# Kernel optimization log

Measured on AMD Instinct MI355X. Metric: run time of the kernel, lower is better.

Reference implementation:

```python
import jax, jax.numpy as jnp
import numpy as np

NUM_CAV = 62000            # CAVs in the ragged batch
K = 3                      # past frames per object


def _counts():
    # deterministic ragged counts in [1, 31]; sum = 2000 * 496 = 992000 objects
    return ((np.arange(NUM_CAV) % 31) + 1).astype(np.int32)


def setup_inputs() -> dict:
    key = jax.random.key(0)
    k1, k2 = jax.random.split(key)
    counts = _counts()
    n_obj = int(counts.sum())  # 992000
    # [N, 3, 7] past 7-dof boxes; only [..., :2] (x, y) is used
    past_k_object_bbx = jax.random.normal(k1, (n_obj, K, 7), dtype=jnp.float32) * 10.0
    # strictly increasing timestamps per CAV so frame-to-frame dt != 0
    dt = jax.random.uniform(k2, (NUM_CAV, K), dtype=jnp.float32, minval=0.05, maxval=0.2)
    past_k_time_interval = jnp.cumsum(dt, axis=1).reshape(-1)  # flat, view(-1,3) compatible
    past_k_object_cav_num = jnp.asarray(counts)
    return {
        'past_k_object_bbx': past_k_object_bbx,
        'past_k_time_interval': past_k_time_interval,
        'past_k_object_cav_num': past_k_object_cav_num,
    }


def reference(past_k_object_bbx, past_k_time_interval, past_k_object_cav_num):
    # Faithful vectorization of extract_date_backup1 (j-indexed replicate loop ==
    # repeat_interleave of per-CAV time rows to per-object rows).
    n_obj = past_k_object_bbx.shape[0]
    # time grid per CAV, reversed so index -1 is the most recent frame
    td = jnp.flip(past_k_time_interval.reshape(-1, K), axis=1)        # [C, 3]
    coords = jnp.flip(past_k_object_bbx[:, :, :2], axis=1)           # [N, 3, 2]
    coords = coords - coords[:, -1:, :]                               # normalize to last frame
    # ragged row replication -> gather via cumulative offsets
    offsets = jnp.cumsum(past_k_object_cav_num)                       # [C]
    cav_idx = jnp.searchsorted(offsets, jnp.arange(n_obj), side='right')
    td_rep = td[cav_idx]                                              # [N, 3]
    td_norm = td_rep - td_rep[:, -1:]                                  # [N, 3]
    dt = td_rep[:, 1:] - td_rep[:, :-1]                                # [N, 2] (time_encode)
    distance = coords[:, 1:, :] - coords[:, :-1, :]                    # [N, 2, 2]
    speed = distance / dt[..., None]                                   # [N, 2, 2]
    obj_input = jnp.concatenate([distance, speed], axis=-1)[None]      # [1, N, 2, 4]
    # linear extrapolation of last motion to t = 0 (the 'query')
    last_len = td_norm[:, -1] - td_norm[:, -2]                          # [N]
    safe_len = jnp.where(last_len == 0, jnp.float32(1.0), last_len)
    extrap = coords[:, -1, :] + (coords[:, -1, :] - coords[:, -2, :]) * (-td_rep[:, -1:]) / safe_len[:, None]
    query = jnp.where((last_len == 0)[:, None], jnp.float32(0.0), extrap).reshape(1, n_obj, 1, 2)
    target_time_diff = -td_rep[:, -1]                                  # [N]
    time_encode = dt                                                   # [N, 2]
    return obj_input, query, time_encode, target_time_diff
```

## Files before the change

### kernel.cpp

```cpp
#include <hip/hip_runtime.h>
#include <limits.h>
#include <stdint.h>

#define SCAN_BS 256
#define OBJ_BS  256
#define SLAB_F  (OBJ_BS * 21)
#define SLAB_CH (SLAB_F / 256)

__device__ __forceinline__ void gload_lds16(const void* g, void* l) {
    __builtin_amdgcn_global_load_lds(
        (const __attribute__((address_space(1))) uint32_t*)g,
        (__attribute__((address_space(3))) uint32_t*)l, 16, 0, 0);
}

__global__ __launch_bounds__(SCAN_BS) void chunk_sum_kernel(
    const int* __restrict__ counts, int C, int* __restrict__ chunkSum) {

    __shared__ int ws[SCAN_BS / 64];
    const int tid  = threadIdx.x;
    const int lane = tid & 63;
    const int wid  = tid >> 6;
    const int gid  = blockIdx.x * SCAN_BS + tid;

    int v = (gid < C) ? counts[gid] : 0;
    #pragma unroll
    for (int o = 32; o > 0; o >>= 1) v += __shfl_down(v, o, 64);
    if (lane == 0) ws[wid] = v;
    __syncthreads();
    if (tid == 0) chunkSum[blockIdx.x] = ws[0] + ws[1] + ws[2] + ws[3];
}

__global__ __launch_bounds__(SCAN_BS) void scan_emit_kernel(
    const int* __restrict__ counts, const int* __restrict__ chunkSum,
    int C, int nb, int* __restrict__ offsets, int* __restrict__ blockCav) {

    __shared__ int cw[SCAN_BS / 64];
    __shared__ int wv[SCAN_BS / 64];

    const int tid  = threadIdx.x;
    const int lane = tid & 63;
    const int wid  = tid >> 6;
    const int b    = blockIdx.x;
    const int gid  = b * SCAN_BS + tid;

    int cs = 0;
    for (int j = tid; j < b; j += SCAN_BS) cs += chunkSum[j];
    #pragma unroll
    for (int o = 32; o > 0; o >>= 1) cs += __shfl_down(cs, o, 64);

    const int v = (gid < C) ? counts[gid] : 0;
    int inc = v;
    #pragma unroll
    for (int o = 1; o < 64; o <<= 1) {
        int t = __shfl_up(inc, o, 64);
        if (lane >= o) inc += t;
    }

    if (lane == 0)  cw[wid] = cs;
    if (lane == 63) wv[wid] = inc;
    __syncthreads();

    int base = 0;
    #pragma unroll
    for (int w = 0; w < SCAN_BS / 64; ++w) {
        base += cw[w];
        if (w < wid) base += wv[w];
    }

    if (gid < C) {
        const int end = base + inc;
        offsets[gid] = end;
        const int start = end - v;
        int s0 = ((start + OBJ_BS - 1) / OBJ_BS) * OBJ_BS;
        for (int s = s0; s < end; s += OBJ_BS) blockCav[s / OBJ_BS] = gid;
    }
}


__global__ __launch_bounds__(OBJ_BS) void motion_kernel(
    const float* __restrict__ bbx, const float* __restrict__ tint,
    const int* __restrict__ offsets, const int* __restrict__ blockCav,
    int C, int N, float* __restrict__ out) {

    __shared__ __align__(16) float sb[SLAB_F];
    __shared__ int   soff[OBJ_BS + 1];
    __shared__ float st[3 * (OBJ_BS + 1)];

    const int tid  = threadIdx.x;
    const int lane = tid & 63;
    const int wid  = tid >> 6;
    const long long blockStart = (long long)blockIdx.x * OBJ_BS;
    const int nObjBlk = (int)min((long long)OBJ_BS, (long long)N - blockStart);

    const int c_lo = blockCav[blockIdx.x];

    const float* gsrc = bbx + blockStart * 21;
    if (nObjBlk == OBJ_BS) {
        #pragma unroll
        for (int ch = wid; ch < SLAB_CH; ch += 4)
            gload_lds16((const void*)(gsrc + ch * 256 + lane * 4), (void*)(sb + ch * 256));
    } else {
        const int nElem = nObjBlk * 21;
        for (int k = tid; k < nElem; k += OBJ_BS) sb[k] = gsrc[k];
    }

    const int c = c_lo + tid;
    const int offv = (c < C) ? offsets[c] : INT_MAX;
    int off_last = INT_MAX;
    if (tid == 0) {
        int c2 = c_lo + OBJ_BS;
        off_last = (c2 < C) ? offsets[c2] : INT_MAX;
    }
    const int base3 = 3 * c_lo;
    const int lim3  = 3 * C - base3;
    const float tv0 = (tid < lim3)       ? tint[base3 + tid]       : 0.0f;
    const float tv1 = (tid + 256 < lim3) ? tint[base3 + tid + 256] : 0.0f;
    const float tv2 = (tid + 512 < lim3) ? tint[base3 + tid + 512] : 0.0f;
    float tv3 = 0.0f;
    if (tid < 3 && tid + 768 < lim3) tv3 = tint[base3 + tid + 768];

    soff[tid] = offv;
    if (tid == 0) soff[OBJ_BS] = off_last;
    st[tid]       = tv0;
    st[tid + 256] = tv1;
    st[tid + 512] = tv2;
    if (tid < 3) st[tid + 768] = tv3;

    __syncthreads();

    if (tid >= nObjBlk) return;
    const int i = (int)(blockStart + tid);

    int lo = 0, hi = OBJ_BS + 1;
    while (lo < hi) {
        int mid = (lo + hi) >> 1;
        if (soff[mid] > i) hi = mid; else lo = mid + 1;
    }
    const int j = lo;
    const float t0 = st[3 * j + 0];
    const float t1 = st[3 * j + 1];
    const float t2 = st[3 * j + 2];

    const float dt0 = t1 - t2;
    const float dt1 = t0 - t1;

    const float* b = sb + tid * 21;
    const float x0 = b[0],  y0 = b[1];
    const float x1 = b[7],  y1 = b[8];
    const float x2 = b[14], y2 = b[15];

    const float c0x = x2 - x0, c0y = y2 - y0;
    const float c1x = x1 - x0, c1y = y1 - y0;

    const float d0x = c1x - c0x, d0y = c1y - c0y;
    const float d1x = 0.0f - c1x, d1y = 0.0f - c1y;

    const float s0x = d0x / dt0, s0y = d0y / dt0;
    const float s1x = d1x / dt1, s1y = d1y / dt1;

    const float last_len = 0.0f - (t1 - t0);
    const float safe_len = (last_len == 0.0f) ? 1.0f : last_len;
    const float exx = ((0.0f - c1x) * (0.0f - t0)) / safe_len;
    const float exy = ((0.0f - c1y) * (0.0f - t0)) / safe_len;
    const float qx = (last_len == 0.0f) ? 0.0f : exx;
    const float qy = (last_len == 0.0f) ? 0.0f : exy;

    const size_t Ns = (size_t)N;
    float4* oi = (float4*)out;
    oi[(size_t)i * 2 + 0] = make_float4(d0x, d0y, s0x, s0y);
    oi[(size_t)i * 2 + 1] = make_float4(d1x, d1y, s1x, s1y);

    float2* q  = (float2*)(out + 8 * Ns);
    q[i] = make_float2(qx, qy);

    float2* te = (float2*)(out + 10 * Ns);
    te[i] = make_float2(dt0, dt1);

    out[12 * Ns + (size_t)i] = 0.0f - t0;
}


extern "C" void kernel_launch(void* const* d_in, const int* in_sizes, int n_in,
                              void* d_out, int out_size, void* d_ws, size_t ws_size,
                              hipStream_t stream) {
    const float* bbx  = (const float*)d_in[0];
    const float* tint = (const float*)d_in[1];
    const int*   cnt  = (const int*)d_in[2];
    float* out = (float*)d_out;

    const int N = in_sizes[0] / 21;
    const int C = in_sizes[2];

    const int nb  = (C + SCAN_BS - 1) / SCAN_BS;
    const int nob = (N + OBJ_BS - 1) / OBJ_BS;

    int* offsets  = (int*)d_ws;
    int* blockCav = offsets + C + 64;
    int* chunkSum = blockCav + nob + 64;

    chunk_sum_kernel<<<nb, SCAN_BS, 0, stream>>>(cnt, C, chunkSum);
    scan_emit_kernel<<<nb, SCAN_BS, 0, stream>>>(cnt, chunkSum, C, nb, offsets, blockCav);
    motion_kernel<<<nob, OBJ_BS, 0, stream>>>(bbx, tint, offsets, blockCav, C, N, out);
}
```

Measured before the change: 34.55 us.

## Resolve CAV lookup per wavefront using shuffle search and per-wave LDS slabs

The motion kernel now maps each 64-object wavefront to its own LDS slab and a wave-level start CAV index, replacing the block-wide shared offset and time tables. The CAV search becomes a 6-step shuffle-based binary search over 64 offsets held in registers, and the three time values are read directly from global memory per object. This removes the shared staging and long LDS binary search, but the scan kernel now writes four times as many start indices. The tail wave falls back to a global binary search.

```diff
diff --git a/kernel.cpp b/kernel.cpp
--- a/kernel.cpp
+++ b/kernel.cpp
@@ -2,15 +2,20 @@
 #include <limits.h>
 #include <stdint.h>
 
-#define SCAN_BS 256
-#define OBJ_BS  256
-#define SLAB_F  (OBJ_BS * 21)
-#define SLAB_CH (SLAB_F / 256)
+#define SCAN_BS  256
+#define MOT_BS   256
+#define WAVE_OBJ 64
+#define WSLAB_F  (WAVE_OBJ * 21)
 
 __device__ __forceinline__ void gload_lds16(const void* g, void* l) {
     __builtin_amdgcn_global_load_lds(
         (const __attribute__((address_space(1))) uint32_t*)g,
         (__attribute__((address_space(3))) uint32_t*)l, 16, 0, 0);
+}
+__device__ __forceinline__ void gload_lds4(const void* g, void* l) {
+    __builtin_amdgcn_global_load_lds(
+        (const __attribute__((address_space(1))) uint32_t*)g,
+        (__attribute__((address_space(3))) uint32_t*)l, 4, 0, 0);
 }
 
 __global__ __launch_bounds__(SCAN_BS) void chunk_sum_kernel(
@@ -32,7 +37,7 @@
 
 __global__ __launch_bounds__(SCAN_BS) void scan_emit_kernel(
     const int* __restrict__ counts, const int* __restrict__ chunkSum,
-    int C, int nb, int* __restrict__ offsets, int* __restrict__ blockCav) {
+    int C, int* __restrict__ offsets, int* __restrict__ waveCav) {
 
     __shared__ int cw[SCAN_BS / 64];
     __shared__ int wv[SCAN_BS / 64];
@@ -71,83 +76,83 @@
         const int end = base + inc;
         offsets[gid] = end;
         const int start = end - v;
-        int s0 = ((start + OBJ_BS - 1) / OBJ_BS) * OBJ_BS;
-        for (int s = s0; s < end; s += OBJ_BS) blockCav[s / OBJ_BS] = gid;
-    }
-}
-
-
-__global__ __launch_bounds__(OBJ_BS) void motion_kernel(
+        int s0 = ((start + WAVE_OBJ - 1) / WAVE_OBJ) * WAVE_OBJ;
+        for (int s = s0; s < end; s += WAVE_OBJ) waveCav[s / WAVE_OBJ] = gid;
+    }
+}
+
+
+__global__ __launch_bounds__(MOT_BS) void motion_kernel(
     const float* __restrict__ bbx, const float* __restrict__ tint,
-    const int* __restrict__ offsets, const int* __restrict__ blockCav,
+    const int* __restrict__ offsets, const int* __restrict__ waveCav,
     int C, int N, float* __restrict__ out) {
 
-    __shared__ __align__(16) float sb[SLAB_F];
-    __shared__ int   soff[OBJ_BS + 1];
-    __shared__ float st[3 * (OBJ_BS + 1)];
+    __shared__ __align__(16) float sb[(MOT_BS / 64) * WSLAB_F];
 
     const int tid  = threadIdx.x;
     const int lane = tid & 63;
     const int wid  = tid >> 6;
-    const long long blockStart = (long long)blockIdx.x * OBJ_BS;
-    const int nObjBlk = (int)min((long long)OBJ_BS, (long long)N - blockStart);
-
-    const int c_lo = blockCav[blockIdx.x];
-
-    const float* gsrc = bbx + blockStart * 21;
-    if (nObjBlk == OBJ_BS) {
+    const int w    = blockIdx.x * (MOT_BS / 64) + wid;
+    const int objBase = w * WAVE_OBJ;
+    const int i = objBase + lane;
+    const bool fullWave = (objBase + WAVE_OBJ <= N);
+
+    int cav = 0;
+    float t0 = 1.0f, t1 = 1.0f, t2 = 1.0f;
+
+    if (fullWave) {
+        const int c0 = waveCav[w];
+        float* slab = sb + wid * WSLAB_F;
+        const float* gw = bbx + (size_t)objBase * 21;
         #pragma unroll
-        for (int ch = wid; ch < SLAB_CH; ch += 4)
-            gload_lds16((const void*)(gsrc + ch * 256 + lane * 4), (void*)(sb + ch * 256));
+        for (int ch = 0; ch < 5; ++ch)
+            gload_lds16((const void*)(gw + ch * 256 + lane * 4), (void*)(slab + ch * 256));
+        gload_lds4((const void*)(gw + 1280 + lane), (void*)(slab + 1280));
+
+        const int cc   = c0 + lane;
+        const int offv = (cc < C) ? offsets[cc] : INT_MAX;
+
+        int k = 0;
+        #pragma unroll
+        for (int s = 32; s >= 1; s >>= 1) {
+            const int vt = __shfl(offv, k + s - 1, 64);
+            if (vt <= i) k += s;
+        }
+        cav = c0 + k;
+
+        t0 = tint[3 * cav + 0];
+        t1 = tint[3 * cav + 1];
+        t2 = tint[3 * cav + 2];
+    }
+
+    __syncthreads();
+
+    if (i >= N) return;
+
+    float x0, y0, x1, y1, x2, y2;
+    if (fullWave) {
+        const float* bp = sb + wid * WSLAB_F + lane * 21;
+        x0 = bp[0];  y0 = bp[1];
+        x1 = bp[7];  y1 = bp[8];
+        x2 = bp[14]; y2 = bp[15];
     } else {
-        const int nElem = nObjBlk * 21;
-        for (int k = tid; k < nElem; k += OBJ_BS) sb[k] = gsrc[k];
-    }
-
-    const int c = c_lo + tid;
-    const int offv = (c < C) ? offsets[c] : INT_MAX;
-    int off_last = INT_MAX;
-    if (tid == 0) {
-        int c2 = c_lo + OBJ_BS;
-        off_last = (c2 < C) ? offsets[c2] : INT_MAX;
-    }
-    const int base3 = 3 * c_lo;
-    const int lim3  = 3 * C - base3;
-    const float tv0 = (tid < lim3)       ? tint[base3 + tid]       : 0.0f;
-    const float tv1 = (tid + 256 < lim3) ? tint[base3 + tid + 256] : 0.0f;
-    const float tv2 = (tid + 512 < lim3) ? tint[base3 + tid + 512] : 0.0f;
-    float tv3 = 0.0f;
-    if (tid < 3 && tid + 768 < lim3) tv3 = tint[base3 + tid + 768];
-
-    soff[tid] = offv;
-    if (tid == 0) soff[OBJ_BS] = off_last;
-    st[tid]       = tv0;
-    st[tid + 256] = tv1;
-    st[tid + 512] = tv2;
-    if (tid < 3) st[tid + 768] = tv3;
-
-    __syncthreads();
-
-    if (tid >= nObjBlk) return;
-    const int i = (int)(blockStart + tid);
-
-    int lo = 0, hi = OBJ_BS + 1;
-    while (lo < hi) {
-        int mid = (lo + hi) >> 1;
-        if (soff[mid] > i) hi = mid; else lo = mid + 1;
-    }
-    const int j = lo;
-    const float t0 = st[3 * j + 0];
-    const float t1 = st[3 * j + 1];
-    const float t2 = st[3 * j + 2];
+        int lo = 0, hi = C;
+        while (lo < hi) {
+            const int mid = (lo + hi) >> 1;
+            if (offsets[mid] > i) hi = mid; else lo = mid + 1;
+        }
+        cav = lo;
+        t0 = tint[3 * cav + 0];
+        t1 = tint[3 * cav + 1];
+        t2 = tint[3 * cav + 2];
+        const float* bp = bbx + (size_t)i * 21;
+        x0 = bp[0];  y0 = bp[1];
+        x1 = bp[7];  y1 = bp[8];
+        x2 = bp[14]; y2 = bp[15];
+    }
 
     const float dt0 = t1 - t2;
     const float dt1 = t0 - t1;
-
-    const float* b = sb + tid * 21;
-    const float x0 = b[0],  y0 = b[1];
-    const float x1 = b[7],  y1 = b[8];
-    const float x2 = b[14], y2 = b[15];
 
     const float c0x = x2 - x0, c0y = y2 - y0;
     const float c1x = x1 - x0, c1y = y1 - y0;
@@ -191,14 +196,15 @@
     const int N = in_sizes[0] / 21;
     const int C = in_sizes[2];
 
-    const int nb  = (C + SCAN_BS - 1) / SCAN_BS;
-    const int nob = (N + OBJ_BS - 1) / OBJ_BS;
+    const int nb     = (C + SCAN_BS - 1) / SCAN_BS;
+    const int nWaves = (N + WAVE_OBJ - 1) / WAVE_OBJ;
+    const int nob    = (nWaves * WAVE_OBJ + MOT_BS - 1) / MOT_BS;
 
     int* offsets  = (int*)d_ws;
-    int* blockCav = offsets + C + 64;
-    int* chunkSum = blockCav + nob + 64;
+    int* waveCav  = offsets + C + 64;
+    int* chunkSum = waveCav + nWaves + 64;
 
     chunk_sum_kernel<<<nb, SCAN_BS, 0, stream>>>(cnt, C, chunkSum);
-    scan_emit_kernel<<<nb, SCAN_BS, 0, stream>>>(cnt, chunkSum, C, nb, offsets, blockCav);
-    motion_kernel<<<nob, OBJ_BS, 0, stream>>>(bbx, tint, offsets, blockCav, C, N, out);
-}
+    scan_emit_kernel<<<nb, SCAN_BS, 0, stream>>>(cnt, chunkSum, C, offsets, waveCav);
+    motion_kernel<<<nob, MOT_BS, 0, stream>>>(bbx, tint, offsets, waveCav, C, N, out);
+}
```

After: 34.39 us. About the same (-0.4%).
